# Performance work log

Hardware: AMD Instinct MI355X
Metric: run time of the kernel (lower is better)

The kernel has to match this reference:

```python
import jax, jax.numpy as jnp
import numpy as np

B, D, H, L, M = 32768, 768, 1024, 256, 32  # batch, input_dim, hidden, latent, context_memory_size
LN_EPS = 1e-5


def _ln(x, g, b):
    mu = jnp.mean(x, axis=-1, keepdims=True)
    var = jnp.mean(jnp.square(x - mu), axis=-1, keepdims=True)
    return (x - mu) * jax.lax.rsqrt(var + LN_EPS) * g + b


def _lrelu(x):
    return jnp.where(x >= 0, x, 0.2 * x)


def setup_inputs() -> dict:
    key = jax.random.key(0)
    ks = jax.random.split(key, 32)
    w = lambda k, shp: jax.random.normal(k, shp, jnp.float32) * (0.7 / np.sqrt(shp[-1]))
    return {
        "x": jax.random.normal(ks[0], (B, D), jnp.float32),
        "eps": jax.random.normal(ks[1], (B, L), jnp.float32),
        # encoder
        "enc_w1": w(ks[2], (H, D)), "enc_b1": jnp.zeros((H,), jnp.float32),
        "ln1_g": jnp.ones((H,), jnp.float32), "ln1_b": jnp.zeros((H,), jnp.float32),
        "enc_w2": w(ks[3], (H, H)), "enc_b2": jnp.zeros((H,), jnp.float32),
        "ln2_g": jnp.ones((H,), jnp.float32), "ln2_b": jnp.zeros((H,), jnp.float32),
        "mu_w": w(ks[4], (L, H)), "mu_b": jnp.zeros((L,), jnp.float32),
        "lv_w": w(ks[5], (L, H)), "lv_b": jnp.zeros((L,), jnp.float32),
        # decoder
        "di_w": w(ks[6], (H, L)), "di_b": jnp.zeros((H,), jnp.float32),
        "dec_w1": w(ks[7], (H, H)), "dec_b1": jnp.zeros((H,), jnp.float32),
        "dln1_g": jnp.ones((H,), jnp.float32), "dln1_b": jnp.zeros((H,), jnp.float32),
        "dec_w2": w(ks[8], (2 * H, H)), "dec_b2": jnp.zeros((2 * H,), jnp.float32),
        "dln2_g": jnp.ones((2 * H,), jnp.float32), "dln2_b": jnp.zeros((2 * H,), jnp.float32),
        "dec_w3": w(ks[9], (D, 2 * H)), "dec_b3": jnp.zeros((D,), jnp.float32),
        "ctx_mem": jax.random.normal(ks[10], (M, L), jnp.float32),
    }


def reference(x, eps, enc_w1, enc_b1, ln1_g, ln1_b, enc_w2, enc_b2, ln2_g, ln2_b,
              mu_w, mu_b, lv_w, lv_b, di_w, di_b, dec_w1, dec_b1, dln1_g, dln1_b,
              dec_w2, dec_b2, dln2_g, dln2_b, dec_w3, dec_b3, ctx_mem):
    # encode (Dropout is identity in eval mode)
    h = _lrelu(_ln(x @ enc_w1.T + enc_b1, ln1_g, ln1_b))
    h = _lrelu(_ln(h @ enc_w2.T + enc_b2, ln2_g, ln2_b))
    mu = h @ mu_w.T + mu_b
    logvar = h @ lv_w.T + lv_b
    # reparameterize
    z = mu + eps * jnp.exp(0.5 * logvar)
    # enhanced decode: context-memory attention
    attn = jax.nn.softmax(z @ ctx_mem.T, axis=-1)        # [B, M]
    z_enh = z + 0.1 * (attn @ ctx_mem)                   # [B, L]
    d = _lrelu(z_enh @ di_w.T + di_b)
    d = _lrelu(_ln(d @ dec_w1.T + dec_b1, dln1_g, dln1_b))
    d = _lrelu(_ln(d @ dec_w2.T + dec_b2, dln2_g, dln2_b))  # [B, 2H]
    reconstructed = d @ dec_w3.T + dec_b3                # [B, D]
    return reconstructed, mu, logvar
```

## Files before the change

kernel.cpp:

```cpp
#include <hip/hip_runtime.h>
#include <stdint.h>

#define DEV __device__ __forceinline__

typedef short bf16x8 __attribute__((ext_vector_type(8)));
typedef float f32x4 __attribute__((ext_vector_type(4)));

DEV ushort f2bf(float x) {
  uint32_t u = __builtin_bit_cast(uint32_t, x);
  return (ushort)((u + 0x7fffu + ((u >> 16) & 1u)) >> 16);
}
DEV float bf2f(ushort h) { return __builtin_bit_cast(float, (uint32_t)h << 16); }

DEV void gload_lds16(const void* g, void* l) {
  __builtin_amdgcn_global_load_lds((const __attribute__((address_space(1))) uint32_t*)g,
                                   (__attribute__((address_space(3))) uint32_t*)l, 16, 0, 0);
}

template <int EPI>
__global__ __launch_bounds__(256, 2) void gemm_bt(
    const ushort* __restrict__ A, int lda, const ushort* __restrict__ W, int ldb,
    void* __restrict__ Cv, int ldc, const float* __restrict__ bias, int K) {
  __shared__ ushort As[128 * 64];
  __shared__ ushort Bs[128 * 64];
  const int t = threadIdx.x;
  const int l = t & 63;
  const int w = t >> 6;
  const int wr = w >> 1, wc = w & 1;
  const int rowBase = blockIdx.y << 7;
  const int colBase = blockIdx.x << 7;

  const int cr = l >> 3;
  const int ccol = ((l & 7) ^ cr) << 3;
  const ushort* aS = A + (size_t)(rowBase + cr) * lda + ccol;
  const ushort* bS = W + (size_t)(colBase + cr) * ldb + ccol;

  f32x4 acc[4][4] = {};

  const int nk = K >> 6;
  for (int kt = 0; kt < nk; ++kt) {
    if (kt) __syncthreads();
    const int k0 = kt << 6;
#pragma unroll
    for (int c4 = 0; c4 < 4; ++c4) {
      const int ch = (w << 2) + c4;
      gload_lds16(aS + (size_t)(ch << 3) * lda + k0, (char*)As + (ch << 10));
      gload_lds16(bS + (size_t)(ch << 3) * ldb + k0, (char*)Bs + (ch << 10));
    }
    __syncthreads();

    bf16x8 af[2][4], bw[2][4];
    const int koff = (l >> 4) << 4;
#pragma unroll
    for (int mi = 0; mi < 4; ++mi) {
      const int r = (wr << 6) + (mi << 4) + (l & 15);
      const char* rp = (const char*)As + (r << 7);
      const int sw = (r & 7) << 4;
      af[0][mi] = *(const bf16x8*)(rp + (koff ^ sw));
      af[1][mi] = *(const bf16x8*)(rp + ((64 + koff) ^ sw));
    }
#pragma unroll
    for (int ni = 0; ni < 4; ++ni) {
      const int r = (wc << 6) + (ni << 4) + (l & 15);
      const char* rp = (const char*)Bs + (r << 7);
      const int sw = (r & 7) << 4;
      bw[0][ni] = *(const bf16x8*)(rp + (koff ^ sw));
      bw[1][ni] = *(const bf16x8*)(rp + ((64 + koff) ^ sw));
    }
#pragma unroll
    for (int kk = 0; kk < 2; ++kk)
#pragma unroll
      for (int mi = 0; mi < 4; ++mi)
#pragma unroll
        for (int ni = 0; ni < 4; ++ni)
          acc[mi][ni] = __builtin_amdgcn_mfma_f32_16x16x32_bf16(
              af[kk][mi], bw[kk][ni], acc[mi][ni], 0, 0, 0);
  }

  const int orow = (l >> 4) << 2;
  const int ocol = l & 15;
#pragma unroll
  for (int ni = 0; ni < 4; ++ni) {
    const int col = colBase + (wc << 6) + (ni << 4) + ocol;
    const float bv = bias[col];
#pragma unroll
    for (int mi = 0; mi < 4; ++mi) {
      const int row0 = rowBase + (wr << 6) + (mi << 4) + orow;
#pragma unroll
      for (int j = 0; j < 4; ++j) {
        float v = acc[mi][ni][j] + bv;
        if (EPI == 2) v = v >= 0.f ? v : 0.2f * v;
        const size_t idx = (size_t)(row0 + j) * ldc + col;
        if (EPI == 0)
          ((float*)Cv)[idx] = v;
        else
          ((ushort*)Cv)[idx] = f2bf(v);
      }
    }
  }
}

template <int N>
__global__ __launch_bounds__(256) void ln_lrelu(ushort* __restrict__ buf,
                                                const float* __restrict__ g,
                                                const float* __restrict__ b) {
  constexpr int E = N / 256;
  const int t = threadIdx.x;
  ushort* p = buf + (size_t)blockIdx.x * N + t * E;
  ushort us[E];
  *(ushort4*)&us[0] = *(const ushort4*)p;
  if constexpr (E == 8) *(ushort4*)&us[4] = *(const ushort4*)(p + 4);
  float f[E], s = 0.f, sq = 0.f;
#pragma unroll
  for (int j = 0; j < E; ++j) {
    f[j] = bf2f(us[j]);
    s += f[j];
    sq += f[j] * f[j];
  }
#pragma unroll
  for (int d = 32; d; d >>= 1) {
    s += __shfl_xor(s, d);
    sq += __shfl_xor(sq, d);
  }
  __shared__ float red[8];
  if ((t & 63) == 0) {
    red[(t >> 6) * 2] = s;
    red[(t >> 6) * 2 + 1] = sq;
  }
  __syncthreads();
  s = red[0] + red[2] + red[4] + red[6];
  sq = red[1] + red[3] + red[5] + red[7];
  const float mean = s * (1.f / N);
  const float rstd = rsqrtf(sq * (1.f / N) - mean * mean + 1e-5f);
  const float* gp = g + t * E;
  const float* bp = b + t * E;
#pragma unroll
  for (int j = 0; j < E; ++j) {
    float y = (f[j] - mean) * rstd * gp[j] + bp[j];
    y = y >= 0.f ? y : 0.2f * y;
    us[j] = f2bf(y);
  }
  *(ushort4*)p = *(ushort4*)&us[0];
  if constexpr (E == 8) *(ushort4*)(p + 4) = *(ushort4*)&us[4];
}

__global__ __launch_bounds__(256) void reparam_attn(
    const float* __restrict__ mu, const float* __restrict__ lv,
    const float* __restrict__ eps, const float* __restrict__ ctx,
    ushort* __restrict__ zb) {
  __shared__ float ctx_lds[32][257];
  __shared__ float z_lds[4][256];
  __shared__ float w_lds[4][32];
  const int t = threadIdx.x;
  for (int i = t; i < 32 * 256; i += 256) ctx_lds[i >> 8][i & 255] = ctx[i];
  __syncthreads();
  const int l = t & 63, wv = t >> 6;
  const int gw = blockIdx.x * 4 + wv;
  const int m = l & 31, half = l >> 5;
  for (int it = 0; it < 8; ++it) {
    const int r = gw + 4096 * it;
    const size_t base = (size_t)r * 256;
    float z[4];
#pragma unroll
    for (int j = 0; j < 4; ++j) {
      const int c = l + 64 * j;
      z[j] = mu[base + c] + eps[base + c] * __expf(0.5f * lv[base + c]);
      z_lds[wv][c] = z[j];
    }
    __syncthreads();
    float s = 0.f;
#pragma unroll 4
    for (int i2 = 0; i2 < 128; ++i2) {
      const int c = half * 128 + i2;
      s += ctx_lds[m][c] * z_lds[wv][c];
    }
    s += __shfl_xor(s, 32);
    float mx = s;
#pragma unroll
    for (int d2 = 16; d2; d2 >>= 1) mx = fmaxf(mx, __shfl_xor(mx, d2));
    const float e = __expf(s - mx);
    float sm = e;
#pragma unroll
    for (int d2 = 16; d2; d2 >>= 1) sm += __shfl_xor(sm, d2);
    w_lds[wv][m] = e / sm;
    __syncthreads();
#pragma unroll
    for (int j = 0; j < 4; ++j) {
      const int c = l + 64 * j;
      float a = 0.f;
#pragma unroll 8
      for (int mm = 0; mm < 32; ++mm) a += w_lds[wv][mm] * ctx_lds[mm][c];
      zb[base + c] = f2bf(z[j] + 0.1f * a);
    }
    __syncthreads();
  }
}

struct ConvArgs {
  const float* src[9];
  ushort* dst[9];
  int n4[9];
};
__global__ __launch_bounds__(256) void conv_bf16(ConvArgs a) {
  const int y = blockIdx.y;
  const float4* s = (const float4*)a.src[y];
  ushort4* d = (ushort4*)a.dst[y];
  const int n4 = a.n4[y];
  const int stride = gridDim.x * 256;
  for (int i = blockIdx.x * 256 + threadIdx.x; i < n4; i += stride) {
    float4 v = s[i];
    ushort4 o;
    o.x = f2bf(v.x); o.y = f2bf(v.y); o.z = f2bf(v.z); o.w = f2bf(v.w);
    d[i] = o;
  }
}

extern "C" void kernel_launch(void* const* d_in, const int* in_sizes, int n_in,
                              void* d_out, int out_size, void* d_ws, size_t ws_size,
                              hipStream_t stream) {
  constexpr size_t NB = 32768, ND = 768, NL = 256;

  const float* x = (const float*)d_in[0];
  const float* eps = (const float*)d_in[1];

  char* ws = (char*)d_ws;
  ushort* XB = (ushort*)(ws + 0);
  ushort* T1 = (ushort*)(ws + 0);
  ushort* T2 = (ushort*)(ws + 67108864ull);
  ushort* T3 = (ushort*)(ws + 67108864ull);
  ushort* ZB = (ushort*)(ws + 134217728ull);
  ushort* WB = (ushort*)(ws + 201326592ull);

  ushort* w1 = WB;
  ushort* w2 = w1 + 786432;
  ushort* wmu = w2 + 1048576;
  ushort* wlv = wmu + 262144;
  ushort* wdi = wlv + 262144;
  ushort* wd1 = wdi + 262144;
  ushort* wd2 = wd1 + 1048576;
  ushort* wd3 = wd2 + 2097152;

  ConvArgs ca;
  ca.src[0] = x;                      ca.dst[0] = XB;  ca.n4[0] = (int)(NB * ND / 4);
  ca.src[1] = (const float*)d_in[2];  ca.dst[1] = w1;  ca.n4[1] = 786432 / 4;
  ca.src[2] = (const float*)d_in[6];  ca.dst[2] = w2;  ca.n4[2] = 1048576 / 4;
  ca.src[3] = (const float*)d_in[10]; ca.dst[3] = wmu; ca.n4[3] = 262144 / 4;
  ca.src[4] = (const float*)d_in[12]; ca.dst[4] = wlv; ca.n4[4] = 262144 / 4;
  ca.src[5] = (const float*)d_in[14]; ca.dst[5] = wdi; ca.n4[5] = 262144 / 4;
  ca.src[6] = (const float*)d_in[16]; ca.dst[6] = wd1; ca.n4[6] = 1048576 / 4;
  ca.src[7] = (const float*)d_in[20]; ca.dst[7] = wd2; ca.n4[7] = 2097152 / 4;
  ca.src[8] = (const float*)d_in[24]; ca.dst[8] = wd3; ca.n4[8] = 1572864 / 4;
  conv_bf16<<<dim3(1024, 9), 256, 0, stream>>>(ca);

  float* out = (float*)d_out;
  float* mu_o = out + NB * ND;
  float* lv_o = mu_o + NB * NL;

  gemm_bt<1><<<dim3(8, 256), 256, 0, stream>>>(XB, 768, w1, 768, T2, 1024,
                                               (const float*)d_in[3], 768);
  ln_lrelu<1024><<<32768, 256, 0, stream>>>(T2, (const float*)d_in[4], (const float*)d_in[5]);
  gemm_bt<1><<<dim3(8, 256), 256, 0, stream>>>(T2, 1024, w2, 1024, T1, 1024,
                                               (const float*)d_in[7], 1024);
  ln_lrelu<1024><<<32768, 256, 0, stream>>>(T1, (const float*)d_in[8], (const float*)d_in[9]);
  gemm_bt<0><<<dim3(2, 256), 256, 0, stream>>>(T1, 1024, wmu, 1024, mu_o, 256,
                                               (const float*)d_in[11], 1024);
  gemm_bt<0><<<dim3(2, 256), 256, 0, stream>>>(T1, 1024, wlv, 1024, lv_o, 256,
                                               (const float*)d_in[13], 1024);
  reparam_attn<<<1024, 256, 0, stream>>>(mu_o, lv_o, eps, (const float*)d_in[26], ZB);
  gemm_bt<2><<<dim3(8, 256), 256, 0, stream>>>(ZB, 256, wdi, 256, T2, 1024,
                                               (const float*)d_in[15], 256);
  gemm_bt<1><<<dim3(8, 256), 256, 0, stream>>>(T2, 1024, wd1, 1024, T1, 1024,
                                               (const float*)d_in[17], 1024);
  ln_lrelu<1024><<<32768, 256, 0, stream>>>(T1, (const float*)d_in[18], (const float*)d_in[19]);
  gemm_bt<1><<<dim3(16, 256), 256, 0, stream>>>(T1, 1024, wd2, 1024, T3, 2048,
                                                (const float*)d_in[21], 1024);
  ln_lrelu<2048><<<32768, 256, 0, stream>>>(T3, (const float*)d_in[22], (const float*)d_in[23]);
  gemm_bt<0><<<dim3(6, 256), 256, 0, stream>>>(T3, 2048, wd3, 2048, out, 768,
                                               (const float*)d_in[25], 2048);
}
```

Before: 1.113 ms.

## Replace 128x128 GEMM with double-buffered 256x256 8-wave pipelined GEMM

Measured after the change: 1.111 ms. About the same (-0.2%).

```diff
diff --git a/kernel.cpp b/kernel.cpp
--- a/kernel.cpp
+++ b/kernel.cpp
@@ -17,84 +17,172 @@
                                    (__attribute__((address_space(3))) uint32_t*)l, 16, 0, 0);
 }
 
+DEV bf16x8 ldv(const void* p) { return *(const bf16x8*)p; }
+
+#define BARRIER __builtin_amdgcn_s_barrier()
+#define SCHED0 __builtin_amdgcn_sched_barrier(0)
+#define PRIO1 __builtin_amdgcn_s_setprio(1)
+#define PRIO0 __builtin_amdgcn_s_setprio(0)
+#define LGKM0                                        \
+  do {                                               \
+    asm volatile("s_waitcnt lgkmcnt(0)" ::: "memory"); \
+    SCHED0;                                          \
+  } while (0)
+
+#define MFMA16(MH, NH, F, Bq)                                                   \
+  _Pragma("unroll") for (int mi = 0; mi < 4; ++mi) {                            \
+    _Pragma("unroll") for (int ni = 0; ni < 2; ++ni) {                          \
+      acc[(MH)*4 + mi][(NH)*2 + ni] = __builtin_amdgcn_mfma_f32_16x16x32_bf16(  \
+          F[mi][0], Bq[ni][0], acc[(MH)*4 + mi][(NH)*2 + ni], 0, 0, 0);         \
+      acc[(MH)*4 + mi][(NH)*2 + ni] = __builtin_amdgcn_mfma_f32_16x16x32_bf16(  \
+          F[mi][1], Bq[ni][1], acc[(MH)*4 + mi][(NH)*2 + ni], 0, 0, 0);         \
+    }                                                                           \
+  }
+
 template <int EPI>
-__global__ __launch_bounds__(256, 2) void gemm_bt(
+__global__ __launch_bounds__(512, 2) void g256(
     const ushort* __restrict__ A, int lda, const ushort* __restrict__ W, int ldb,
-    void* __restrict__ Cv, int ldc, const float* __restrict__ bias, int K) {
-  __shared__ ushort As[128 * 64];
-  __shared__ ushort Bs[128 * 64];
+    void* __restrict__ Cv, long ldc, const float* __restrict__ bias,
+    const float* __restrict__ bias2, long splitStride, int K) {
+  __shared__ ushort As[2][256 * 64];
+  __shared__ ushort Bs[2][256 * 64];
   const int t = threadIdx.x;
   const int l = t & 63;
   const int w = t >> 6;
-  const int wr = w >> 1, wc = w & 1;
-  const int rowBase = blockIdx.y << 7;
-  const int colBase = blockIdx.x << 7;
-
-  const int cr = l >> 3;
-  const int ccol = ((l & 7) ^ cr) << 3;
-  const ushort* aS = A + (size_t)(rowBase + cr) * lda + ccol;
-  const ushort* bS = W + (size_t)(colBase + cr) * ldb + ccol;
-
-  f32x4 acc[4][4] = {};
+  const int wm = w >> 2, wn = w & 3;
+
+  const int nwg = gridDim.x * gridDim.y;
+  int bid = blockIdx.y * gridDim.x + blockIdx.x;
+  const int cpx = nwg >> 3;
+  bid = (bid & 7) * cpx + (bid >> 3);
+  const int bx = bid % gridDim.x;
+  const int by = bid / gridDim.x;
+  const long rowBase = (long)by << 8;
+  const int colBase = bx << 8;
+
+  const int srow = l >> 3;
+  const int scol = ((l & 7) ^ srow) << 3;
+  const ushort* aB = A + (size_t)(rowBase + srow) * lda + scol;
+  const ushort* bB = W + (size_t)(colBase + srow) * ldb + scol;
+  const int aC0 = wm * 16 + wn * 2;
+  const int aC2 = aC0 + 8;
+  const int bC0 = (wn >> 1) * 16 + (wm * 2 + (wn & 1)) * 4;
+
+  const int fro = l & 15;
+  const int o0 = (((l >> 4) << 4)) ^ ((l & 7) << 4);
+  const int o1 = (64 + ((l >> 4) << 4)) ^ ((l & 7) << 4);
+
+#define STG_A(KT1, CH) \
+  gload_lds16(aB + (size_t)((CH) << 3) * lda + ((size_t)(KT1) << 6), \
+              (char*)As[(KT1) & 1] + ((CH) << 10))
+#define STG_B(KT1, CH) \
+  gload_lds16(bB + (size_t)((CH) << 3) * ldb + ((size_t)(KT1) << 6), \
+              (char*)Bs[(KT1) & 1] + ((CH) << 10))
+
+  STG_A(0, aC0); STG_A(0, aC0 + 1);
+  STG_B(0, bC0); STG_B(0, bC0 + 1); STG_B(0, bC0 + 2); STG_B(0, bC0 + 3);
+  STG_A(0, aC2); STG_A(0, aC2 + 1);
+  asm volatile("s_waitcnt vmcnt(2)" ::: "memory");
+  BARRIER;
 
   const int nk = K >> 6;
+  f32x4 acc[8][4] = {};
+  bf16x8 af[4][2], b0[2][2], b1[2][2];
+
   for (int kt = 0; kt < nk; ++kt) {
-    if (kt) __syncthreads();
-    const int k0 = kt << 6;
-#pragma unroll
-    for (int c4 = 0; c4 < 4; ++c4) {
-      const int ch = (w << 2) + c4;
-      gload_lds16(aS + (size_t)(ch << 3) * lda + k0, (char*)As + (ch << 10));
-      gload_lds16(bS + (size_t)(ch << 3) * ldb + k0, (char*)Bs + (ch << 10));
-    }
-    __syncthreads();
-
-    bf16x8 af[2][4], bw[2][4];
-    const int koff = (l >> 4) << 4;
+    const int p = kt & 1;
+    const bool stage = (kt + 1) < nk;
+    const int kt1 = kt + 1;
+    const char* Ap = (const char*)As[p] + (wm * 128 + fro) * 128;
+    const char* Bp = (const char*)Bs[p] + (wn * 64 + fro) * 128;
+
 #pragma unroll
     for (int mi = 0; mi < 4; ++mi) {
-      const int r = (wr << 6) + (mi << 4) + (l & 15);
-      const char* rp = (const char*)As + (r << 7);
-      const int sw = (r & 7) << 4;
-      af[0][mi] = *(const bf16x8*)(rp + (koff ^ sw));
-      af[1][mi] = *(const bf16x8*)(rp + ((64 + koff) ^ sw));
-    }
-#pragma unroll
-    for (int ni = 0; ni < 4; ++ni) {
-      const int r = (wc << 6) + (ni << 4) + (l & 15);
-      const char* rp = (const char*)Bs + (r << 7);
-      const int sw = (r & 7) << 4;
-      bw[0][ni] = *(const bf16x8*)(rp + (koff ^ sw));
-      bw[1][ni] = *(const bf16x8*)(rp + ((64 + koff) ^ sw));
-    }
-#pragma unroll
-    for (int kk = 0; kk < 2; ++kk)
-#pragma unroll
-      for (int mi = 0; mi < 4; ++mi)
-#pragma unroll
-        for (int ni = 0; ni < 4; ++ni)
-          acc[mi][ni] = __builtin_amdgcn_mfma_f32_16x16x32_bf16(
-              af[kk][mi], bw[kk][ni], acc[mi][ni], 0, 0, 0);
-  }
+      af[mi][0] = ldv(Ap + mi * 2048 + o0);
+      af[mi][1] = ldv(Ap + mi * 2048 + o1);
+    }
+#pragma unroll
+    for (int ni = 0; ni < 2; ++ni) {
+      b0[ni][0] = ldv(Bp + ni * 2048 + o0);
+      b0[ni][1] = ldv(Bp + ni * 2048 + o1);
+    }
+    if (stage) { STG_A(kt1, aC0); STG_A(kt1, aC0 + 1); }
+    BARRIER;
+    LGKM0;
+    PRIO1;
+    MFMA16(0, 0, af, b0);
+    SCHED0;
+    PRIO0;
+    BARRIER;
+
+#pragma unroll
+    for (int ni = 0; ni < 2; ++ni) {
+      b1[ni][0] = ldv(Bp + 4096 + ni * 2048 + o0);
+      b1[ni][1] = ldv(Bp + 4096 + ni * 2048 + o1);
+    }
+    if (stage) { STG_B(kt1, bC0); STG_B(kt1, bC0 + 1); }
+    BARRIER;
+    LGKM0;
+    PRIO1;
+    MFMA16(0, 1, af, b1);
+    SCHED0;
+    PRIO0;
+    if (stage) asm volatile("s_waitcnt vmcnt(4)" ::: "memory");
+    else       asm volatile("s_waitcnt vmcnt(0)" ::: "memory");
+    BARRIER;
+
+#pragma unroll
+    for (int mi = 0; mi < 4; ++mi) {
+      af[mi][0] = ldv(Ap + 8192 + mi * 2048 + o0);
+      af[mi][1] = ldv(Ap + 8192 + mi * 2048 + o1);
+    }
+    if (stage) { STG_B(kt1, bC0 + 2); STG_B(kt1, bC0 + 3); }
+    BARRIER;
+    LGKM0;
+    PRIO1;
+    MFMA16(1, 1, af, b1);
+    SCHED0;
+    PRIO0;
+    BARRIER;
+
+    if (stage) { STG_A(kt1, aC2); STG_A(kt1, aC2 + 1); }
+    BARRIER;
+    SCHED0;
+    PRIO1;
+    MFMA16(1, 0, af, b0);
+    SCHED0;
+    PRIO0;
+    if (stage) asm volatile("s_waitcnt vmcnt(2)" ::: "memory");
+    BARRIER;
+  }
+#undef STG_A
+#undef STG_B
 
   const int orow = (l >> 4) << 2;
   const int ocol = l & 15;
 #pragma unroll
   for (int ni = 0; ni < 4; ++ni) {
-    const int col = colBase + (wc << 6) + (ni << 4) + ocol;
-    const float bv = bias[col];
-#pragma unroll
-    for (int mi = 0; mi < 4; ++mi) {
-      const int row0 = rowBase + (wr << 6) + (mi << 4) + orow;
+    const int col = colBase + wn * 64 + ni * 16 + ocol;
+    float bv;
+    if (EPI == 3)
+      bv = (col < 256) ? bias[col] : bias2[col - 256];
+    else
+      bv = bias[col];
+#pragma unroll
+    for (int mi = 0; mi < 8; ++mi) {
+      const long row0 = rowBase + wm * 128 + mi * 16 + orow;
 #pragma unroll
       for (int j = 0; j < 4; ++j) {
         float v = acc[mi][ni][j] + bv;
         if (EPI == 2) v = v >= 0.f ? v : 0.2f * v;
-        const size_t idx = (size_t)(row0 + j) * ldc + col;
-        if (EPI == 0)
+        if (EPI == 0) {
+          ((float*)Cv)[(row0 + j) * ldc + col] = v;
+        } else if (EPI == 3) {
+          const long idx = (row0 + j) * 256 + (col & 255) + (long)(col >> 8) * splitStride;
           ((float*)Cv)[idx] = v;
-        else
-          ((ushort*)Cv)[idx] = f2bf(v);
+        } else {
+          ((ushort*)Cv)[(row0 + j) * ldc + col] = f2bf(v);
+        }
       }
     }
   }
@@ -256,25 +344,26 @@
   float* mu_o = out + NB * ND;
   float* lv_o = mu_o + NB * NL;
 
-  gemm_bt<1><<<dim3(8, 256), 256, 0, stream>>>(XB, 768, w1, 768, T2, 1024,
-                                               (const float*)d_in[3], 768);
+  const long SPLIT = (long)NB * 256;
+
+  g256<1><<<dim3(4, 128), 512, 0, stream>>>(XB, 768, w1, 768, T2, 1024,
+                                            (const float*)d_in[3], nullptr, 0, 768);
   ln_lrelu<1024><<<32768, 256, 0, stream>>>(T2, (const float*)d_in[4], (const float*)d_in[5]);
-  gemm_bt<1><<<dim3(8, 256), 256, 0, stream>>>(T2, 1024, w2, 1024, T1, 1024,
-                                               (const float*)d_in[7], 1024);
+  g256<1><<<dim3(4, 128), 512, 0, stream>>>(T2, 1024, w2, 1024, T1, 1024,
+                                            (const float*)d_in[7], nullptr, 0, 1024);
   ln_lrelu<1024><<<32768, 256, 0, stream>>>(T1, (const float*)d_in[8], (const float*)d_in[9]);
-  gemm_bt<0><<<dim3(2, 256), 256, 0, stream>>>(T1, 1024, wmu, 1024, mu_o, 256,
-                                               (const float*)d_in[11], 1024);
-  gemm_bt<0><<<dim3(2, 256), 256, 0, stream>>>(T1, 1024, wlv, 1024, lv_o, 256,
-                                               (const float*)d_in[13], 1024);
+  g256<3><<<dim3(2, 128), 512, 0, stream>>>(T1, 1024, wmu, 1024, mu_o, 256,
+                                            (const float*)d_in[11], (const float*)d_in[13],
+                                            SPLIT, 1024);
   reparam_attn<<<1024, 256, 0, stream>>>(mu_o, lv_o, eps, (const float*)d_in[26], ZB);
-  gemm_bt<2><<<dim3(8, 256), 256, 0, stream>>>(ZB, 256, wdi, 256, T2, 1024,
-                                               (const float*)d_in[15], 256);
-  gemm_bt<1><<<dim3(8, 256), 256, 0, stream>>>(T2, 1024, wd1, 1024, T1, 1024,
-                                               (const float*)d_in[17], 1024);
+  g256<2><<<dim3(4, 128), 512, 0, stream>>>(ZB, 256, wdi, 256, T2, 1024,
+                                            (const float*)d_in[15], nullptr, 0, 256);
+  g256<1><<<dim3(4, 128), 512, 0, stream>>>(T2, 1024, wd1, 1024, T1, 1024,
+                                            (const float*)d_in[17], nullptr, 0, 1024);
   ln_lrelu<1024><<<32768, 256, 0, stream>>>(T1, (const float*)d_in[18], (const float*)d_in[19]);
-  gemm_bt<1><<<dim3(16, 256), 256, 0, stream>>>(T1, 1024, wd2, 1024, T3, 2048,
-                                                (const float*)d_in[21], 1024);
+  g256<1><<<dim3(8, 128), 512, 0, stream>>>(T1, 1024, wd2, 1024, T3, 2048,
+                                            (const float*)d_in[21], nullptr, 0, 1024);
   ln_lrelu<2048><<<32768, 256, 0, stream>>>(T3, (const float*)d_in[22], (const float*)d_in[23]);
-  gemm_bt<0><<<dim3(6, 256), 256, 0, stream>>>(T3, 2048, wd3, 2048, out, 768,
-                                               (const float*)d_in[25], 2048);
-}
+  g256<0><<<dim3(3, 128), 512, 0, stream>>>(T3, 2048, wd3, 2048, out, 768,
+                                            (const float*)d_in[25], nullptr, 0, 2048);
+}
```

## Fuse LayerNorm into GEMM prologue/epilogue and merge mu/logvar GEMMs

Applied to the files above, without the earlier changes.

Measured after the change: 1.248 ms. 12.1% more time.

```diff
diff --git a/kernel.cpp b/kernel.cpp
--- a/kernel.cpp
+++ b/kernel.cpp
@@ -17,10 +17,13 @@
                                    (__attribute__((address_space(3))) uint32_t*)l, 16, 0, 0);
 }
 
-template <int EPI>
+template <int EPI, int LNIN, int STATS>
 __global__ __launch_bounds__(256, 2) void gemm_bt(
     const ushort* __restrict__ A, int lda, const ushort* __restrict__ W, int ldb,
-    void* __restrict__ Cv, int ldc, const float* __restrict__ bias, int K) {
+    void* __restrict__ Cv, long ldc, const float* __restrict__ bias,
+    const float* __restrict__ bias2, long splitStride,
+    const float2* __restrict__ stIn, const float* __restrict__ gam,
+    const float* __restrict__ bet, float invN, float* __restrict__ stOut, int K) {
   __shared__ ushort As[128 * 64];
   __shared__ ushort Bs[128 * 64];
   const int t = threadIdx.x;
@@ -32,8 +35,10 @@
 
   const int cr = l >> 3;
   const int ccol = ((l & 7) ^ cr) << 3;
+  const int lcol = (l & 7) << 3;
   const ushort* aS = A + (size_t)(rowBase + cr) * lda + ccol;
   const ushort* bS = W + (size_t)(colBase + cr) * ldb + ccol;
+  const int wofs = cr * 128 + (((l & 7) << 4) ^ (cr << 4));
 
   f32x4 acc[4][4] = {};
 
@@ -44,8 +49,44 @@
 #pragma unroll
     for (int c4 = 0; c4 < 4; ++c4) {
       const int ch = (w << 2) + c4;
-      gload_lds16(aS + (size_t)(ch << 3) * lda + k0, (char*)As + (ch << 10));
       gload_lds16(bS + (size_t)(ch << 3) * ldb + k0, (char*)Bs + (ch << 10));
+    }
+    if constexpr (LNIN) {
+      const float4 g0 = *(const float4*)(gam + k0 + lcol);
+      const float4 g1 = *(const float4*)(gam + k0 + lcol + 4);
+      const float4 be0 = *(const float4*)(bet + k0 + lcol);
+      const float4 be1 = *(const float4*)(bet + k0 + lcol + 4);
+      bf16x8 raw[4];
+      float2 st[4];
+#pragma unroll
+      for (int c4 = 0; c4 < 4; ++c4) {
+        const int ch = (w << 2) + c4;
+        const int ar = rowBase + (ch << 3) + cr;
+        raw[c4] = *(const bf16x8*)(A + (size_t)ar * lda + k0 + lcol);
+        st[c4] = stIn[ar];
+      }
+      const float gv[8] = {g0.x, g0.y, g0.z, g0.w, g1.x, g1.y, g1.z, g1.w};
+      const float bv[8] = {be0.x, be0.y, be0.z, be0.w, be1.x, be1.y, be1.z, be1.w};
+#pragma unroll
+      for (int c4 = 0; c4 < 4; ++c4) {
+        const int ch = (w << 2) + c4;
+        const float mean = st[c4].x * invN;
+        const float rstd = rsqrtf(st[c4].y * invN - mean * mean + 1e-5f);
+        bf16x8 o;
+#pragma unroll
+        for (int j = 0; j < 8; ++j) {
+          float v = (bf2f((ushort)raw[c4][j]) - mean) * rstd * gv[j] + bv[j];
+          v = v >= 0.f ? v : 0.2f * v;
+          o[j] = (short)f2bf(v);
+        }
+        *(bf16x8*)((char*)As + (ch << 10) + wofs) = o;
+      }
+    } else {
+#pragma unroll
+      for (int c4 = 0; c4 < 4; ++c4) {
+        const int ch = (w << 2) + c4;
+        gload_lds16(aS + (size_t)(ch << 3) * lda + k0, (char*)As + (ch << 10));
+      }
     }
     __syncthreads();
 
@@ -79,69 +120,57 @@
 
   const int orow = (l >> 4) << 2;
   const int ocol = l & 15;
+  float ps[4][4] = {};
+  float pq[4][4] = {};
 #pragma unroll
   for (int ni = 0; ni < 4; ++ni) {
     const int col = colBase + (wc << 6) + (ni << 4) + ocol;
-    const float bv = bias[col];
+    float bv;
+    if constexpr (EPI == 3)
+      bv = (col < 256) ? bias[col] : bias2[col - 256];
+    else
+      bv = bias[col];
 #pragma unroll
     for (int mi = 0; mi < 4; ++mi) {
       const int row0 = rowBase + (wr << 6) + (mi << 4) + orow;
 #pragma unroll
       for (int j = 0; j < 4; ++j) {
         float v = acc[mi][ni][j] + bv;
-        if (EPI == 2) v = v >= 0.f ? v : 0.2f * v;
-        const size_t idx = (size_t)(row0 + j) * ldc + col;
-        if (EPI == 0)
+        if constexpr (STATS) {
+          ps[mi][j] += v;
+          pq[mi][j] += v * v;
+        }
+        if constexpr (EPI == 2) v = v >= 0.f ? v : 0.2f * v;
+        if constexpr (EPI == 0) {
+          ((float*)Cv)[(long)(row0 + j) * ldc + col] = v;
+        } else if constexpr (EPI == 3) {
+          const long idx =
+              (long)(row0 + j) * 256 + (col & 255) + (long)(col >> 8) * splitStride;
           ((float*)Cv)[idx] = v;
-        else
-          ((ushort*)Cv)[idx] = f2bf(v);
-      }
-    }
-  }
-}
-
-template <int N>
-__global__ __launch_bounds__(256) void ln_lrelu(ushort* __restrict__ buf,
-                                                const float* __restrict__ g,
-                                                const float* __restrict__ b) {
-  constexpr int E = N / 256;
-  const int t = threadIdx.x;
-  ushort* p = buf + (size_t)blockIdx.x * N + t * E;
-  ushort us[E];
-  *(ushort4*)&us[0] = *(const ushort4*)p;
-  if constexpr (E == 8) *(ushort4*)&us[4] = *(const ushort4*)(p + 4);
-  float f[E], s = 0.f, sq = 0.f;
-#pragma unroll
-  for (int j = 0; j < E; ++j) {
-    f[j] = bf2f(us[j]);
-    s += f[j];
-    sq += f[j] * f[j];
-  }
-#pragma unroll
-  for (int d = 32; d; d >>= 1) {
-    s += __shfl_xor(s, d);
-    sq += __shfl_xor(sq, d);
-  }
-  __shared__ float red[8];
-  if ((t & 63) == 0) {
-    red[(t >> 6) * 2] = s;
-    red[(t >> 6) * 2 + 1] = sq;
-  }
-  __syncthreads();
-  s = red[0] + red[2] + red[4] + red[6];
-  sq = red[1] + red[3] + red[5] + red[7];
-  const float mean = s * (1.f / N);
-  const float rstd = rsqrtf(sq * (1.f / N) - mean * mean + 1e-5f);
-  const float* gp = g + t * E;
-  const float* bp = b + t * E;
-#pragma unroll
-  for (int j = 0; j < E; ++j) {
-    float y = (f[j] - mean) * rstd * gp[j] + bp[j];
-    y = y >= 0.f ? y : 0.2f * y;
-    us[j] = f2bf(y);
-  }
-  *(ushort4*)p = *(ushort4*)&us[0];
-  if constexpr (E == 8) *(ushort4*)(p + 4) = *(ushort4*)&us[4];
+        } else {
+          ((ushort*)Cv)[(long)(row0 + j) * ldc + col] = f2bf(v);
+        }
+      }
+    }
+  }
+  if constexpr (STATS) {
+#pragma unroll
+    for (int mi = 0; mi < 4; ++mi)
+#pragma unroll
+      for (int j = 0; j < 4; ++j) {
+        float s = ps[mi][j], q = pq[mi][j];
+#pragma unroll
+        for (int d = 1; d < 16; d <<= 1) {
+          s += __shfl_xor(s, d);
+          q += __shfl_xor(q, d);
+        }
+        if ((l & 15) == 0) {
+          const int r = rowBase + (wr << 6) + (mi << 4) + orow + j;
+          atomicAdd(stOut + 2 * r, s);
+          atomicAdd(stOut + 2 * r + 1, q);
+        }
+      }
+  }
 }
 
 __global__ __launch_bounds__(256) void reparam_attn(
@@ -230,6 +259,11 @@
   ushort* T3 = (ushort*)(ws + 67108864ull);
   ushort* ZB = (ushort*)(ws + 134217728ull);
   ushort* WB = (ushort*)(ws + 201326592ull);
+  float2* ST = (float2*)(ws + 216006656ull);
+  float2* st1 = ST;
+  float2* st2 = st1 + 32768;
+  float2* st3 = st2 + 32768;
+  float2* st4 = st3 + 32768;
 
   ushort* w1 = WB;
   ushort* w2 = w1 + 786432;
@@ -239,6 +273,8 @@
   ushort* wd1 = wdi + 262144;
   ushort* wd2 = wd1 + 1048576;
   ushort* wd3 = wd2 + 2097152;
+
+  hipMemsetAsync(ST, 0, 4 * 32768 * sizeof(float2), stream);
 
   ConvArgs ca;
   ca.src[0] = x;                      ca.dst[0] = XB;  ca.n4[0] = (int)(NB * ND / 4);
@@ -255,26 +291,29 @@
   float* out = (float*)d_out;
   float* mu_o = out + NB * ND;
   float* lv_o = mu_o + NB * NL;
-
-  gemm_bt<1><<<dim3(8, 256), 256, 0, stream>>>(XB, 768, w1, 768, T2, 1024,
-                                               (const float*)d_in[3], 768);
-  ln_lrelu<1024><<<32768, 256, 0, stream>>>(T2, (const float*)d_in[4], (const float*)d_in[5]);
-  gemm_bt<1><<<dim3(8, 256), 256, 0, stream>>>(T2, 1024, w2, 1024, T1, 1024,
-                                               (const float*)d_in[7], 1024);
-  ln_lrelu<1024><<<32768, 256, 0, stream>>>(T1, (const float*)d_in[8], (const float*)d_in[9]);
-  gemm_bt<0><<<dim3(2, 256), 256, 0, stream>>>(T1, 1024, wmu, 1024, mu_o, 256,
-                                               (const float*)d_in[11], 1024);
-  gemm_bt<0><<<dim3(2, 256), 256, 0, stream>>>(T1, 1024, wlv, 1024, lv_o, 256,
-                                               (const float*)d_in[13], 1024);
+  const long SPLIT = (long)NB * 256;
+  const float i1024 = 1.0f / 1024.f, i2048 = 1.0f / 2048.f;
+
+  gemm_bt<1, 0, 1><<<dim3(8, 256), 256, 0, stream>>>(
+      XB, 768, w1, 768, T2, 1024, (const float*)d_in[3], nullptr, 0,
+      nullptr, nullptr, nullptr, 0.f, (float*)st1, 768);
+  gemm_bt<1, 1, 1><<<dim3(8, 256), 256, 0, stream>>>(
+      T2, 1024, w2, 1024, T1, 1024, (const float*)d_in[7], nullptr, 0,
+      st1, (const float*)d_in[4], (const float*)d_in[5], i1024, (float*)st2, 1024);
+  gemm_bt<3, 1, 0><<<dim3(4, 256), 256, 0, stream>>>(
+      T1, 1024, wmu, 1024, mu_o, 256, (const float*)d_in[11], (const float*)d_in[13],
+      SPLIT, st2, (const float*)d_in[8], (const float*)d_in[9], i1024, nullptr, 1024);
   reparam_attn<<<1024, 256, 0, stream>>>(mu_o, lv_o, eps, (const float*)d_in[26], ZB);
-  gemm_bt<2><<<dim3(8, 256), 256, 0, stream>>>(ZB, 256, wdi, 256, T2, 1024,
-                                               (const float*)d_in[15], 256);
-  gemm_bt<1><<<dim3(8, 256), 256, 0, stream>>>(T2, 1024, wd1, 1024, T1, 1024,
-                                               (const float*)d_in[17], 1024);
-  ln_lrelu<1024><<<32768, 256, 0, stream>>>(T1, (const float*)d_in[18], (const float*)d_in[19]);
-  gemm_bt<1><<<dim3(16, 256), 256, 0, stream>>>(T1, 1024, wd2, 1024, T3, 2048,
-                                                (const float*)d_in[21], 1024);
-  ln_lrelu<2048><<<32768, 256, 0, stream>>>(T3, (const float*)d_in[22], (const float*)d_in[23]);
-  gemm_bt<0><<<dim3(6, 256), 256, 0, stream>>>(T3, 2048, wd3, 2048, out, 768,
-                                               (const float*)d_in[25], 2048);
-}
+  gemm_bt<2, 0, 0><<<dim3(8, 256), 256, 0, stream>>>(
+      ZB, 256, wdi, 256, T2, 1024, (const float*)d_in[15], nullptr, 0,
+      nullptr, nullptr, nullptr, 0.f, nullptr, 256);
+  gemm_bt<1, 0, 1><<<dim3(8, 256), 256, 0, stream>>>(
+      T2, 1024, wd1, 1024, T1, 1024, (const float*)d_in[17], nullptr, 0,
+      nullptr, nullptr, nullptr, 0.f, (float*)st3, 1024);
+  gemm_bt<1, 1, 1><<<dim3(16, 256), 256, 0, stream>>>(
+      T1, 1024, wd2, 1024, T3, 2048, (const float*)d_in[21], nullptr, 0,
+      st3, (const float*)d_in[18], (const float*)d_in[19], i1024, (float*)st4, 1024);
+  gemm_bt<0, 1, 0><<<dim3(6, 256), 256, 0, stream>>>(
+      T3, 2048, wd3, 2048, out, 768, (const float*)d_in[25], nullptr, 0,
+      st4, (const float*)d_in[22], (const float*)d_in[23], i2048, nullptr, 2048);
+}
```
